# Kernel tuning notes

Measured on AMD Instinct MI355X. Metric: run time of the kernel, lower is better.

Reference implementation:

```python
import jax, jax.numpy as jnp
import numpy as np

GRID = 8
S = GRID * GRID          # 64 tokens
D = 256                  # embed dim
H = 4                    # heads
HD = D // H              # 64 head dim
L = 8                    # depth
EPS = 1.1920929e-07      # torch.finfo(float32).eps (nn.RMSNorm eps=None)
RADIUS = 2.5


def _grid_coords():
    y, x = np.meshgrid(np.arange(GRID), np.arange(GRID), indexing='ij')
    return np.stack([y.ravel(), x.ravel()], axis=1).astype(np.float32)  # [S,2]


def _rope_cos_sin():
    coords = _grid_coords()
    dim_half = HD // 2  # 32
    inv_freq = 1.0 / (10000.0 ** (np.arange(0, dim_half, 2, dtype=np.float32) / dim_half))  # [16]
    fy = coords[:, 0:1] * inv_freq[None, :]   # [S,16]
    fx = coords[:, 1:2] * inv_freq[None, :]   # [S,16]
    freqs = np.concatenate([fy, fx], axis=-1)  # [S,32]
    emb = np.concatenate([freqs, freqs], axis=-1)  # [S,64]
    return jnp.asarray(np.cos(emb)), jnp.asarray(np.sin(emb))


def _local_mask():
    coords = _grid_coords()
    d = np.sqrt(((coords[:, None, :] - coords[None, :, :]) ** 2).sum(-1))
    return jnp.asarray(d < RADIUS)  # [S,S] bool


COS, SIN = _rope_cos_sin()
MASK_LOCAL = _local_mask()
MASK_GLOBAL = jnp.ones((S, S), dtype=bool)


def rms(x):
    return x * jax.lax.rsqrt(jnp.mean(x * x, axis=-1, keepdims=True) + EPS)


def householder_Q(vs):
    # vs: [R, HD]; Q = prod of reflections applied as in the torch loop
    def step(Q, v):
        vn = jnp.sum(v * v) + 1e-08
        return Q - (2.0 / vn) * jnp.outer(v, v @ Q), None
    Q, _ = jax.lax.scan(step, jnp.eye(HD, dtype=vs.dtype), vs)
    return Q


def rotate_half(x):
    x1, x2 = jnp.split(x, 2, axis=-1)
    return jnp.concatenate([-x2, x1], axis=-1)


def block(x, vs_l, wqkv, wout, wg, bg, wmg, bmg, wmo, bmo, mask):
    B = x.shape[0]
    xn = rms(x)
    qkv = xn @ wqkv                                # [B,S,3D]
    q, k, v = jnp.split(qkv, 3, axis=-1)
    q = q.reshape(B, S, H, HD).transpose(0, 2, 1, 3)   # [B,H,S,HD]
    k = k.reshape(B, S, H, HD).transpose(0, 2, 1, 3)
    v = v.reshape(B, S, H, HD).transpose(0, 2, 1, 3)
    Q = householder_Q(vs_l)                        # [HD,HD]
    # inverse rotation, standard RoPE, forward rotation
    q = q @ Q.T
    k = k @ Q.T
    cos = COS[None, None]                          # [1,1,S,HD]
    sin = SIN[None, None]
    q = q * cos + rotate_half(q) * sin
    k = k * cos + rotate_half(k) * sin
    q = q @ Q
    k = k @ Q
    scores = jnp.einsum('bhqd,bhkd->bhqk', q, k) / jnp.sqrt(jnp.float32(HD))
    scores = jnp.where(mask[None, None], scores, -jnp.inf)
    attn = jax.nn.softmax(scores, axis=-1)
    out = jnp.einsum('bhqk,bhkd->bhqd', attn, v)   # [B,H,S,HD]
    out = out.transpose(0, 2, 1, 3).reshape(B, S, D)
    out = out @ wout
    gate = jax.nn.sigmoid(out @ wg + bg)
    x = x + out * gate
    xn = rms(x)
    m = xn @ wmg + bmg                             # [B,S,8D]
    g, val = jnp.split(m, 2, axis=-1)
    x = x + (val * jax.nn.gelu(g, approximate=False)) @ wmo + bmo
    return x


def setup_inputs() -> dict:
    key = jax.random.key(0)
    ks = jax.random.split(key, 20)
    B = 1024
    s = 0.02
    return {
        'z_t': jax.random.normal(ks[0], (B, 3, 16, 16), jnp.float32),
        'logsnr': jax.random.normal(ks[1], (B,), jnp.float32),
        'w_patch_in': jax.random.normal(ks[2], (20, D), jnp.float32) * s,
        'b_patch_in': jnp.zeros((D,), jnp.float32),
        'vs': jax.random.normal(ks[3], (L, HD // 2, HD), jnp.float32) * s,
        'w_qkv': jax.random.normal(ks[4], (L, D, 3 * D), jnp.float32) * s,
        'w_out': jax.random.normal(ks[5], (L, D, D), jnp.float32) * s,
        'w_gate': jax.random.normal(ks[6], (L, D, D), jnp.float32) * s,
        'b_gate': jnp.zeros((L, D), jnp.float32),
        'w_mlp_gate': jax.random.normal(ks[7], (L, D, 8 * D), jnp.float32) * s,
        'b_mlp_gate': jnp.zeros((L, 8 * D), jnp.float32),
        'w_mlp_out': jax.random.normal(ks[8], (L, 4 * D, D), jnp.float32) * s,
        'b_mlp_out': jnp.zeros((L, D), jnp.float32),
        'norm_final_w': jnp.ones((D,), jnp.float32),
        'w_head': jax.random.normal(ks[9], (D, D), jnp.float32) * s,
        'b_head': jnp.zeros((D,), jnp.float32),
        'w_patch_out': jax.random.normal(ks[10], (D, 12), jnp.float32) * s,
        'b_patch_out': jnp.zeros((12,), jnp.float32),
    }


def reference(z_t, logsnr, w_patch_in, b_patch_in, vs, w_qkv, w_out, w_gate, b_gate,
              w_mlp_gate, b_mlp_gate, w_mlp_out, b_mlp_out, norm_final_w,
              w_head, b_head, w_patch_out, b_patch_out):
    B = z_t.shape[0]
    # patchify: [B,3,16,16] -> [B,64,12] (2x2 patches over 8x8 grid)
    patches = z_t.reshape(B, 3, GRID, 2, GRID, 2).transpose(0, 2, 4, 1, 3, 5).reshape(B, S, 12)
    # Fourier features of logsnr: num_bands=4, max_range=40
    freqs = (2.0 * np.pi / 40.0) * (2.0 ** jnp.arange(4, dtype=jnp.float32))
    args = logsnr[:, None] * freqs                 # [B,4]
    spins = jnp.concatenate([jnp.sin(args), jnp.cos(args)], axis=-1)  # [B,8]
    spins = jnp.broadcast_to(spins[:, None, :], (B, S, 8))
    x = jnp.concatenate([patches, spins], axis=-1) @ w_patch_in + b_patch_in  # [B,S,D]
    for i in range(L):
        mask = MASK_GLOBAL if (i + 1) % 4 == 0 else MASK_LOCAL
        x = block(x, vs[i], w_qkv[i], w_out[i], w_gate[i], b_gate[i],
                  w_mlp_gate[i], b_mlp_gate[i], w_mlp_out[i], b_mlp_out[i], mask)
    x = rms(x) * norm_final_w
    out = x @ w_head + b_head
    z = out @ w_patch_out + b_patch_out            # [B,S,12]
    z = z.reshape(B, GRID, GRID, 3, 2, 2).transpose(0, 3, 1, 4, 2, 5).reshape(B, 3, 16, 16)
    return z
```

## Files before the change

kernel.cpp:

```cpp
#include <hip/hip_runtime.h>

#define DEV static __device__ __forceinline__

typedef float f32x4 __attribute__((ext_vector_type(4)));
typedef short s16x8 __attribute__((ext_vector_type(8)));
typedef __bf16 bf16x8 __attribute__((ext_vector_type(8)));

DEV unsigned short f2bf(float f) {
  union { float f; unsigned u; } v; v.f = f;
  unsigned r = v.u + 0x7FFFu + ((v.u >> 16) & 1u);
  return (unsigned short)(r >> 16);
}
DEV float bf2f(unsigned short h) {
  union { unsigned u; float f; } v; v.u = ((unsigned)h) << 16;
  return v.f;
}
DEV void g2l16(const void* g, void* l) {
  __builtin_amdgcn_global_load_lds((const __attribute__((address_space(1))) void*)g,
                                   (__attribute__((address_space(3))) void*)l, 16, 0, 0);
}
DEV f32x4 mfma16(bf16x8 a, bf16x8 b, f32x4 c) {
  return __builtin_amdgcn_mfma_f32_16x16x32_bf16(a, b, c, 0, 0, 0);
}
DEV int xcd_swz(int bid, int nwg) {
  return (bid & 7) * (nwg >> 3) + (bid >> 3);
}
DEV float gelu_t(float g) {
  float y = 0.7978845608028654f * (g + 0.044715f * g * g * g);
  float th = 1.f - 2.f * __builtin_amdgcn_rcpf(1.f + __expf(2.f * y));
  return 0.5f * g * (1.f + th);
}

__global__ void k_house(const float* __restrict__ VS, float* __restrict__ Qg) {
  const int l = blockIdx.x, t = threadIdx.x;
  float Qc[64];
#pragma unroll
  for (int i = 0; i < 64; i++) Qc[i] = (i == t) ? 1.f : 0.f;
  for (int rr = 0; rr < 32; rr++) {
    float vt = VS[(size_t)l * 2048 + rr * 64 + t];
    float vn = vt * vt;
#pragma unroll
    for (int o = 1; o < 64; o <<= 1) vn += __shfl_xor(vn, o, 64);
    float vv[64];
#pragma unroll
    for (int i = 0; i < 64; i++) vv[i] = __shfl(vt, i, 64);
    float w0 = 0.f, w1 = 0.f, w2 = 0.f, w3 = 0.f;
#pragma unroll
    for (int i = 0; i < 64; i += 4) {
      w0 = fmaf(vv[i + 0], Qc[i + 0], w0);
      w1 = fmaf(vv[i + 1], Qc[i + 1], w1);
      w2 = fmaf(vv[i + 2], Qc[i + 2], w2);
      w3 = fmaf(vv[i + 3], Qc[i + 3], w3);
    }
    float c = (2.f / (vn + 1e-8f)) * ((w0 + w1) + (w2 + w3));
#pragma unroll
    for (int i = 0; i < 64; i++) Qc[i] = fmaf(-vv[i], c, Qc[i]);
  }
#pragma unroll
  for (int i = 0; i < 64; i++) Qg[(size_t)l * 4096 + i * 64 + t] = Qc[i];
}

__global__ void k_rope(float* __restrict__ C, float* __restrict__ Sn) {
  int idx = blockIdx.x * 256 + threadIdx.x;
  if (idx >= 4096) return;
  int s = idx >> 6, d = idx & 63;
  int dh = d & 31;
  float coord = (dh < 16) ? (float)(s >> 3) : (float)(s & 7);
  int fi = dh & 15;
  float invf = powf(10000.f, -(float)fi / 16.f);
  float ang = coord * invf;
  C[idx] = cosf(ang);
  Sn[idx] = sinf(ang);
}

__global__ __launch_bounds__(256) void k_fold_qkv(const float* __restrict__ W,
                                                  const float* __restrict__ Qg,
                                                  unsigned short* __restrict__ out) {
  __shared__ float qrows[16 * 64];
  __shared__ float tr[16 * 256];
  const int l = blockIdx.x / 48, ng = blockIdx.x % 48;
  const int n0 = ng * 16, t = threadIdx.x;
  const float* Wl = W + (size_t)l * 256 * 768;
  float res[16];
  if (n0 < 512) {
    int part = n0 >> 8, h = (n0 & 255) >> 6, j0 = n0 & 63;
    for (int i = t; i < 1024; i += 256) {
      int jj = i >> 6, dd = i & 63;
      qrows[i] = Qg[(size_t)l * 4096 + (j0 + jj) * 64 + dd];
    }
    __syncthreads();
    const float* wrow = Wl + (size_t)t * 768 + part * 256 + h * 64;
    float wreg[64];
    for (int d = 0; d < 64; d++) wreg[d] = wrow[d];
    for (int jj = 0; jj < 16; jj++) {
      float a = 0.f;
      for (int d = 0; d < 64; d++) a += wreg[d] * qrows[jj * 64 + d];
      res[jj] = a;
    }
  } else {
    for (int jj = 0; jj < 16; jj++) res[jj] = Wl[(size_t)t * 768 + n0 + jj];
    __syncthreads();
  }
  __syncthreads();
  for (int jj = 0; jj < 16; jj++) tr[jj * 256 + t] = res[jj];
  __syncthreads();
  size_t base = (size_t)l * 196608 + (size_t)(n0 >> 4) * 4096;
  int kb = t >> 3, jn0 = (t & 7) * 2;
  s16x8 w0, w1;
  for (int u = 0; u < 8; u++) w0[u] = (short)f2bf(tr[jn0 * 256 + kb * 8 + u]);
  for (int u = 0; u < 8; u++) w1[u] = (short)f2bf(tr[(jn0 + 1) * 256 + kb * 8 + u]);
  *(s16x8*)(out + base + (size_t)t * 16) = w0;
  *(s16x8*)(out + base + (size_t)t * 16 + 8) = w1;
}

__global__ __launch_bounds__(256) void k_fold_w2(const float* __restrict__ WO,
                                                 const float* __restrict__ WG,
                                                 unsigned short* __restrict__ out) {
  __shared__ float wgs[256 * 16];
  __shared__ float tr[16 * 256];
  const int l = blockIdx.x >> 5, ng = blockIdx.x & 31;
  const int n0 = ng * 16, t = threadIdx.x;
  const float* WOl = WO + (size_t)l * 65536;
  float res[16];
  if (n0 < 256) {
    for (int jj = 0; jj < 16; jj++) res[jj] = WOl[(size_t)t * 256 + n0 + jj];
  } else {
    int c0 = n0 - 256;
    const float* WGl = WG + (size_t)l * 65536;
    for (int i = t; i < 4096; i += 256) {
      int k = i >> 4, c = i & 15;
      wgs[i] = WGl[(size_t)k * 256 + c0 + c];
    }
    __syncthreads();
    float a[16];
    for (int c = 0; c < 16; c++) a[c] = 0.f;
    for (int k = 0; k < 256; k++) {
      float wo = WOl[(size_t)t * 256 + k];
      for (int c = 0; c < 16; c++) a[c] += wo * wgs[k * 16 + c];
    }
    for (int c = 0; c < 16; c++) res[c] = a[c];
  }
  __syncthreads();
  for (int jj = 0; jj < 16; jj++) tr[jj * 256 + t] = res[jj];
  __syncthreads();
  size_t base = (size_t)l * 131072 + (size_t)(n0 >> 4) * 4096;
  int kb = t >> 3, jn0 = (t & 7) * 2;
  s16x8 w0, w1;
  for (int u = 0; u < 8; u++) w0[u] = (short)f2bf(tr[jn0 * 256 + kb * 8 + u]);
  for (int u = 0; u < 8; u++) w1[u] = (short)f2bf(tr[(jn0 + 1) * 256 + kb * 8 + u]);
  *(s16x8*)(out + base + (size_t)t * 16) = w0;
  *(s16x8*)(out + base + (size_t)t * 16 + 8) = w1;
}

__global__ __launch_bounds__(256) void k_conv_wmg(const float* __restrict__ W,
                                                  unsigned short* __restrict__ out) {
  __shared__ float tr[16 * 256];
  const int l = blockIdx.x >> 7, ng = blockIdx.x & 127;
  const int n0 = ng * 16, t = threadIdx.x;
  const float* src = W + (size_t)l * 256 * 2048 + (size_t)t * 2048 + n0;
  for (int j = 0; j < 16; j++) tr[j * 256 + t] = src[j];
  __syncthreads();
  size_t base = (size_t)l * 524288 + (size_t)ng * 4096;
  int kb = t >> 3, jn0 = (t & 7) * 2;
  s16x8 w0, w1;
  for (int u = 0; u < 8; u++) w0[u] = (short)f2bf(tr[jn0 * 256 + kb * 8 + u]);
  for (int u = 0; u < 8; u++) w1[u] = (short)f2bf(tr[(jn0 + 1) * 256 + kb * 8 + u]);
  *(s16x8*)(out + base + (size_t)t * 16) = w0;
  *(s16x8*)(out + base + (size_t)t * 16 + 8) = w1;
}

__global__ __launch_bounds__(256) void k_conv_wmo(const float* __restrict__ W,
                                                  unsigned short* __restrict__ out) {
  __shared__ float tr[16 * 256];
  const int l = blockIdx.x >> 4, ng = blockIdx.x & 15;
  const int n0 = ng * 16, t = threadIdx.x;
  const float* Wl = W + (size_t)l * 1024 * 256;
  size_t base = (size_t)l * 262144 + (size_t)ng * 16384;
  for (int c4 = 0; c4 < 4; c4++) {
    int k0 = c4 * 256;
    for (int j = 0; j < 16; j++) tr[j * 256 + t] = Wl[(size_t)(k0 + t) * 256 + n0 + j];
    __syncthreads();
    int kb = t >> 3, jn0 = (t & 7) * 2;
    s16x8 w0, w1;
    for (int u = 0; u < 8; u++) w0[u] = (short)f2bf(tr[jn0 * 256 + kb * 8 + u]);
    for (int u = 0; u < 8; u++) w1[u] = (short)f2bf(tr[(jn0 + 1) * 256 + kb * 8 + u]);
    *(s16x8*)(out + base + (size_t)(k0 >> 3) * 128 + (size_t)t * 16) = w0;
    *(s16x8*)(out + base + (size_t)(k0 >> 3) * 128 + (size_t)t * 16 + 8) = w1;
    __syncthreads();
  }
}

__global__ __launch_bounds__(256) void k_fold_head(const float* __restrict__ WH,
                                                   const float* __restrict__ BH,
                                                   const float* __restrict__ WPO,
                                                   const float* __restrict__ BPO,
                                                   float* __restrict__ WHP,
                                                   float* __restrict__ BHP) {
  __shared__ float wpos[256 * 12];
  const int t = threadIdx.x;
  for (int i = t; i < 3072; i += 256) wpos[i] = WPO[i];
  __syncthreads();
  float a[12];
  for (int c = 0; c < 12; c++) a[c] = 0.f;
  const float* whrow = WH + (size_t)t * 256;
  for (int k = 0; k < 256; k++) {
    float w = whrow[k];
    for (int c = 0; c < 12; c++) a[c] += w * wpos[k * 12 + c];
  }
  for (int c = 0; c < 12; c++) WHP[t * 12 + c] = a[c];
  if (t < 12) {
    float b = BPO[t];
    for (int k = 0; k < 256; k++) b += BH[k] * wpos[k * 12 + t];
    BHP[t] = b;
  }
}

__global__ __launch_bounds__(256) void k_embed(const float* __restrict__ ZT,
                                               const float* __restrict__ LOGSNR,
                                               const float* __restrict__ WPI,
                                               const float* __restrict__ BPI,
                                               float* __restrict__ X) {
  __shared__ float zb[768];
  __shared__ float sp[8];
  const int b = blockIdx.x, t = threadIdx.x;
  for (int i = t; i < 768; i += 256) zb[i] = ZT[(size_t)b * 768 + i];
  if (t < 8) {
    float freq = 0.15707963267948966f * (float)(1 << (t & 3));
    float a = LOGSNR[b] * freq;
    sp[t] = (t < 4) ? sinf(a) : cosf(a);
  }
  __syncthreads();
  float wc[20];
  for (int j = 0; j < 20; j++) wc[j] = WPI[j * 256 + t];
  float bk = BPI[t];
  for (int s = 0; s < 64; s++) {
    int gy = s >> 3, gx = s & 7;
    float acc = bk;
    for (int j = 0; j < 12; j++) {
      int cch = j >> 2, py = (j >> 1) & 1, px = j & 1;
      acc += zb[cch * 256 + (gy * 2 + py) * 16 + gx * 2 + px] * wc[j];
    }
    for (int j = 0; j < 8; j++) acc += sp[j] * wc[12 + j];
    X[((size_t)b * 64 + s) * 256 + t] = acc;
  }
}

__global__ __launch_bounds__(256) void k_rms(const float* __restrict__ X,
                                             unsigned short* __restrict__ XN) {
  const int m0 = blockIdx.x * 16, t = threadIdx.x;
  const int r = t >> 4, cj = t & 15;
  const float* row = X + (size_t)(m0 + r) * 256 + cj * 16;
  float4 a = *(const float4*)(row);
  float4 b = *(const float4*)(row + 4);
  float4 c = *(const float4*)(row + 8);
  float4 d = *(const float4*)(row + 12);
  float ss = a.x * a.x + a.y * a.y + a.z * a.z + a.w * a.w +
             b.x * b.x + b.y * b.y + b.z * b.z + b.w * b.w +
             c.x * c.x + c.y * c.y + c.z * c.z + c.w * c.w +
             d.x * d.x + d.y * d.y + d.z * d.z + d.w * d.w;
  for (int o = 1; o < 16; o <<= 1) ss += __shfl_xor(ss, o, 64);
  float rq = rsqrtf(ss * (1.f / 256.f) + 1.1920929e-07f);
  s16x8 v0, v1;
  v0[0] = (short)f2bf(a.x * rq); v0[1] = (short)f2bf(a.y * rq);
  v0[2] = (short)f2bf(a.z * rq); v0[3] = (short)f2bf(a.w * rq);
  v0[4] = (short)f2bf(b.x * rq); v0[5] = (short)f2bf(b.y * rq);
  v0[6] = (short)f2bf(b.z * rq); v0[7] = (short)f2bf(b.w * rq);
  v1[0] = (short)f2bf(c.x * rq); v1[1] = (short)f2bf(c.y * rq);
  v1[2] = (short)f2bf(c.z * rq); v1[3] = (short)f2bf(c.w * rq);
  v1[4] = (short)f2bf(d.x * rq); v1[5] = (short)f2bf(d.y * rq);
  v1[6] = (short)f2bf(d.z * rq); v1[7] = (short)f2bf(d.w * rq);
  size_t base = ((size_t)blockIdx.x * 32 + cj * 2) * 128 + r * 8;
  *(s16x8*)(XN + base) = v0;
  *(s16x8*)(XN + base + 128) = v1;
}

template <int KD, int NT, int MODE>
__global__ __launch_bounds__(256) void k_gemm_single(const unsigned short* __restrict__ A,
                                                     const unsigned short* __restrict__ Bw,
                                                     unsigned short* __restrict__ Cout,
                                                     const float* __restrict__ bias,
                                                     float* __restrict__ X) {
  __shared__ unsigned short sm[17408];
  unsigned short* la = sm;
  unsigned short* lb = sm + 4096;
  const int t = threadIdx.x;
  const int lane = t & 63, wv = t >> 6;
  const int swz = xcd_swz(blockIdx.x, gridDim.x);
  const int bm = swz / NT, bn = swz % NT;
  const int m0 = bm * 128, n0 = bn * 128;
  const int wm = wv >> 1, wn = wv & 1;
  constexpr int KB8 = KD >> 3;

  f32x4 acc[4][4];
  f32x4 zz = {0.f, 0.f, 0.f, 0.f};
  for (int i = 0; i < 4; i++)
    for (int j = 0; j < 4; j++) acc[i][j] = zz;

  for (int k0 = 0; k0 < KD; k0 += 32) {
    const int kb0 = k0 >> 3;
    for (int ii = 0; ii < 2; ii++) {
      size_t mg = (size_t)(m0 >> 4) + ii * 4 + wv;
      g2l16(A + (mg * KB8 + kb0) * 128 + lane * 8, la + (ii * 4 + wv) * 512 + lane * 8);
    }
    for (int ii = 0; ii < 2; ii++) {
      size_t ng = (size_t)(n0 >> 4) + ii * 4 + wv;
      g2l16(Bw + (ng * KB8 + kb0) * 128 + lane * 8, lb + (ii * 4 + wv) * 512 + lane * 8);
    }
    __syncthreads();
    bf16x8 af[4], bb[4];
    for (int i = 0; i < 4; i++) af[i] = *(const bf16x8*)(la + (wm * 4 + i) * 512 + lane * 8);
    for (int j = 0; j < 4; j++) bb[j] = *(const bf16x8*)(lb + (wn * 4 + j) * 512 + lane * 8);
    for (int i = 0; i < 4; i++)
      for (int j = 0; j < 4; j++) acc[i][j] = mfma16(af[i], bb[j], acc[i][j]);
    __syncthreads();
  }

  const int lr = lane & 15, lg = lane >> 4;
  if constexpr (MODE == 0) {
    unsigned short* lc = sm;
    for (int i = 0; i < 4; i++)
      for (int j = 0; j < 4; j++)
        for (int e = 0; e < 4; e++) {
          int r = wm * 64 + i * 16 + lg * 4 + e;
          int c = wn * 64 + j * 16 + lr;
          lc[r * 136 + c] = f2bf(acc[i][j][e]);
        }
    __syncthreads();
    for (int p = 0; p < 8; p++) {
      int r = p * 16 + (t >> 4);
      int c = (t & 15) * 8;
      *(s16x8*)(Cout + (size_t)(m0 + r) * (NT * 128) + n0 + c) = *(const s16x8*)(lc + r * 136 + c);
    }
  } else {
    for (int i = 0; i < 4; i++)
      for (int j = 0; j < 4; j++) {
        int c = n0 + wn * 64 + j * 16 + lr;
        float bv = bias[c];
        for (int e = 0; e < 4; e++) {
          int r = m0 + wm * 64 + i * 16 + lg * 4 + e;
          X[(size_t)r * 256 + c] += acc[i][j][e] + bv;
        }
      }
  }
}

template <int KD, int MODE>
__global__ __launch_bounds__(256) void k_gemm_dual(const unsigned short* __restrict__ A,
                                                   const unsigned short* __restrict__ B0,
                                                   const unsigned short* __restrict__ B1,
                                                   const float* __restrict__ bias,
                                                   float* __restrict__ X,
                                                   unsigned short* __restrict__ Hout,
                                                   int NT) {
  __shared__ unsigned short sm[9216];
  unsigned short* la = sm;
  unsigned short* lb0 = sm + 4096;
  unsigned short* lb1 = sm + 6144;
  const int t = threadIdx.x, lane = t & 63, wv = t >> 6;
  const int swz = xcd_swz(blockIdx.x, gridDim.x);
  const int bm = swz / NT, bn = swz % NT;
  const int m0 = bm * 128, n0 = bn * 64;
  constexpr int KB8 = KD >> 3;
  f32x4 acc0[2][4], acc1[2][4];
  f32x4 zz = {0.f, 0.f, 0.f, 0.f};
  for (int i = 0; i < 2; i++)
    for (int j = 0; j < 4; j++) { acc0[i][j] = zz; acc1[i][j] = zz; }

  for (int k0 = 0; k0 < KD; k0 += 32) {
    const int kb0 = k0 >> 3;
    for (int ii = 0; ii < 2; ii++) {
      size_t mg = (size_t)(m0 >> 4) + ii * 4 + wv;
      g2l16(A + (mg * KB8 + kb0) * 128 + lane * 8, la + (ii * 4 + wv) * 512 + lane * 8);
    }
    size_t ng = (size_t)(n0 >> 4) + wv;
    g2l16(B0 + (ng * KB8 + kb0) * 128 + lane * 8, lb0 + wv * 512 + lane * 8);
    g2l16(B1 + (ng * KB8 + kb0) * 128 + lane * 8, lb1 + wv * 512 + lane * 8);
    __syncthreads();
    bf16x8 af[2];
    for (int i = 0; i < 2; i++) af[i] = *(const bf16x8*)(la + (wv * 2 + i) * 512 + lane * 8);
    for (int j = 0; j < 4; j++) {
      bf16x8 b0 = *(const bf16x8*)(lb0 + j * 512 + lane * 8);
      bf16x8 b1 = *(const bf16x8*)(lb1 + j * 512 + lane * 8);
      for (int i = 0; i < 2; i++) {
        acc0[i][j] = mfma16(af[i], b0, acc0[i][j]);
        acc1[i][j] = mfma16(af[i], b1, acc1[i][j]);
      }
    }
    __syncthreads();
  }

  const int lr = lane & 15, lg = lane >> 4;
  if constexpr (MODE == 0) {
    for (int i = 0; i < 2; i++)
      for (int j = 0; j < 4; j++) {
        int c = n0 + j * 16 + lr;
        float bv = bias[c];
        for (int e = 0; e < 4; e++) {
          int r = m0 + wv * 32 + i * 16 + lg * 4 + e;
          float o = acc0[i][j][e];
          float g = acc1[i][j][e] + bv;
          X[(size_t)r * 256 + c] += o * __builtin_amdgcn_rcpf(1.f + __expf(-g));
        }
      }
  } else {
    unsigned short* lc = sm;
    for (int i = 0; i < 2; i++)
      for (int j = 0; j < 4; j++) {
        int cl = j * 16 + lr;
        float bg_ = bias[n0 + cl];
        float bv_ = bias[1024 + n0 + cl];
        for (int e = 0; e < 4; e++) {
          int rl = wv * 32 + i * 16 + lg * 4 + e;
          float g = acc0[i][j][e] + bg_;
          float vv = acc1[i][j][e] + bv_;
          lc[rl * 72 + cl] = f2bf(vv * gelu_t(g));
        }
      }
    __syncthreads();
    for (int it = 0; it < 4; it++) {
      int idx = it * 2048 + t * 8;
      int mg_l = idx >> 10, rem = idx & 1023;
      int kb_l = rem >> 7, r = (rem >> 3) & 15;
      *(s16x8*)(Hout + ((size_t)((m0 >> 4) + mg_l) * 128 + (n0 >> 3) + kb_l) * 128 + r * 8) =
          *(const s16x8*)(lc + (mg_l * 16 + r) * 72 + kb_l * 8);
    }
  }
}

__global__ __launch_bounds__(256) void k_attn(const unsigned short* __restrict__ QKV,
                                              const float* __restrict__ CT,
                                              const float* __restrict__ ST,
                                              unsigned short* __restrict__ AO,
                                              int use_local) {
  __shared__ unsigned short sm[16384];
  unsigned short* qs = sm;
  unsigned short* ks = sm + 4096;
  unsigned short* vt = sm + 8192;
  unsigned short* ps = sm + 12288;
  const int blk = blockIdx.x;
  const int b = blk >> 2, h = blk & 3;
  const int t = threadIdx.x, lane = t & 63, wv = t >> 6;
  const size_t rowbase = (size_t)b * 64 * 768;

  {
    int s = t >> 2, dq = (t & 3) * 8;
    const unsigned short* qrow = QKV + rowbase + (size_t)s * 768 + h * 64;
    s16x8 qlo = *(const s16x8*)(qrow + dq);
    s16x8 qhi = *(const s16x8*)(qrow + dq + 32);
    s16x8 klo = *(const s16x8*)(qrow + 256 + dq);
    s16x8 khi = *(const s16x8*)(qrow + 256 + dq + 32);
    s16x8 oql, oqh, okl, okh;
    for (int e = 0; e < 8; e++) {
      float cl = CT[s * 64 + dq + e], sl = ST[s * 64 + dq + e];
      float ch = CT[s * 64 + dq + 32 + e], sh = ST[s * 64 + dq + 32 + e];
      float ql = bf2f((unsigned short)qlo[e]), qh = bf2f((unsigned short)qhi[e]);
      oql[e] = (short)f2bf((ql * cl - qh * sl) * 0.125f);
      oqh[e] = (short)f2bf((qh * ch + ql * sh) * 0.125f);
      float kl = bf2f((unsigned short)klo[e]), kh = bf2f((unsigned short)khi[e]);
      okl[e] = (short)f2bf(kl * cl - kh * sl);
      okh[e] = (short)f2bf(kh * ch + kl * sh);
    }
    int off_lo = (((s >> 4) * 8 + (dq >> 3)) * 16 + (s & 15)) * 8;
    int off_hi = (((s >> 4) * 8 + (dq >> 3) + 4) * 16 + (s & 15)) * 8;
    *(s16x8*)(qs + off_lo) = oql;
    *(s16x8*)(qs + off_hi) = oqh;
    *(s16x8*)(ks + off_lo) = okl;
    *(s16x8*)(ks + off_hi) = okh;
    int d0 = (t & 3) * 16;
    s16x8 v0 = *(const s16x8*)(qrow + 512 + d0);
    s16x8 v1 = *(const s16x8*)(qrow + 512 + d0 + 8);
    for (int e = 0; e < 8; e++) {
      int d = d0 + e;
      vt[(((d >> 4) * 8 + (s >> 3)) * 16 + (d & 15)) * 8 + (s & 7)] = (unsigned short)v0[e];
      d = d0 + 8 + e;
      vt[(((d >> 4) * 8 + (s >> 3)) * 16 + (d & 15)) * 8 + (s & 7)] = (unsigned short)v1[e];
    }
  }
  __syncthreads();

  f32x4 sc[4];
  f32x4 zz = {0.f, 0.f, 0.f, 0.f};
  for (int j = 0; j < 4; j++) sc[j] = zz;
  for (int kk = 0; kk < 2; kk++) {
    bf16x8 aq = *(const bf16x8*)(qs + wv * 1024 + kk * 512 + lane * 8);
    for (int j = 0; j < 4; j++)
      sc[j] = mfma16(aq, *(const bf16x8*)(ks + j * 1024 + kk * 512 + lane * 8), sc[j]);
  }

  const int lr = lane & 15, lg = lane >> 4;
  for (int e = 0; e < 4; e++) {
    int sq = wv * 16 + lg * 4 + e;
    int yq = sq >> 3, xq = sq & 7;
    float mx = -1e30f;
    float vals[4];
    for (int j = 0; j < 4; j++) {
      int sk = j * 16 + lr;
      float v = sc[j][e];
      if (use_local) {
        int dy = yq - (sk >> 3), dx = xq - (sk & 7);
        if (dy * dy + dx * dx > 6) v = -1e30f;
      }
      vals[j] = v;
      mx = fmaxf(mx, v);
    }
    for (int o = 1; o < 16; o <<= 1) mx = fmaxf(mx, __shfl_xor(mx, o, 64));
    float sum = 0.f;
    for (int j = 0; j < 4; j++) {
      float p = __expf(vals[j] - mx);
      vals[j] = p;
      sum += p;
    }
    for (int o = 1; o < 16; o <<= 1) sum += __shfl_xor(sum, o, 64);
    float inv = __builtin_amdgcn_rcpf(sum);
    for (int j = 0; j < 4; j++) {
      int sk = j * 16 + lr;
      ps[((wv * 8 + (sk >> 3)) * 16 + (sq & 15)) * 8 + (sk & 7)] = f2bf(vals[j] * inv);
    }
  }
  __syncthreads();

  f32x4 oa[4];
  for (int j = 0; j < 4; j++) oa[j] = zz;
  for (int kk = 0; kk < 2; kk++) {
    bf16x8 ap = *(const bf16x8*)(ps + wv * 1024 + kk * 512 + lane * 8);
    for (int j = 0; j < 4; j++)
      oa[j] = mfma16(ap, *(const bf16x8*)(vt + j * 1024 + kk * 512 + lane * 8), oa[j]);
  }
  unsigned short* os = qs + wv * 1024;
  for (int j = 0; j < 4; j++)
    for (int e = 0; e < 4; e++) os[(lg * 4 + e) * 64 + j * 16 + lr] = f2bf(oa[j][e]);
  __syncthreads();
  const size_t obase = ((size_t)(b * 4 + wv) * 32 + h * 8) * 128;
  for (int c = 0; c < 2; c++) {
    int idx = c * 64 + lane;
    int kb = idx >> 4, r = idx & 15;
    *(s16x8*)(AO + obase + (size_t)kb * 128 + r * 8) = *(const s16x8*)(os + r * 64 + kb * 8);
  }
}

__global__ __launch_bounds__(256) void k_head(const float* __restrict__ X,
                                              const float* __restrict__ NW,
                                              const float* __restrict__ WHP,
                                              const float* __restrict__ BHP,
                                              float* __restrict__ OUT) {
  __shared__ float wh[256 * 12];
  __shared__ float nw[256];
  __shared__ float bh[12];
  const int b = blockIdx.x, t = threadIdx.x;
  for (int i = t; i < 3072; i += 256) wh[i] = WHP[i];
  nw[t] = NW[t];
  if (t < 12) bh[t] = BHP[t];
  __syncthreads();
  const int r = t >> 2, qd = t & 3;
  const float* row = X + ((size_t)b * 64 + r) * 256 + qd * 64;
  float ss = 0.f;
  for (int i = 0; i < 64; i++) ss += row[i] * row[i];
  ss += __shfl_xor(ss, 1, 64);
  ss += __shfl_xor(ss, 2, 64);
  float rq = rsqrtf(ss * (1.f / 256.f) + 1.1920929e-07f);
  float accs[12];
  for (int c = 0; c < 12; c++) accs[c] = 0.f;
  for (int i = 0; i < 64; i++) {
    float xf = row[i] * rq * nw[qd * 64 + i];
    const float* wr = wh + (qd * 64 + i) * 12;
    for (int c = 0; c < 12; c++) accs[c] += xf * wr[c];
  }
  for (int c = 0; c < 12; c++) {
    accs[c] += __shfl_xor(accs[c], 1, 64);
    accs[c] += __shfl_xor(accs[c], 2, 64);
  }
  int gy = r >> 3, gx = r & 7;
  for (int u = 0; u < 3; u++) {
    int c = qd * 3 + u;
    float val = accs[c] + bh[c];
    int ch = c >> 2, py = (c >> 1) & 1, px = c & 1;
    OUT[(size_t)b * 768 + ch * 256 + (gy * 2 + py) * 16 + (gx * 2 + px)] = val;
  }
}

extern "C" void kernel_launch(void* const* d_in, const int* in_sizes, int n_in,
                              void* d_out, int out_size, void* d_ws, size_t ws_size,
                              hipStream_t stream) {
  (void)n_in; (void)out_size; (void)ws_size;
  const float* z_t    = (const float*)d_in[0];
  const float* logsnr = (const float*)d_in[1];
  const float* wpi    = (const float*)d_in[2];
  const float* bpi    = (const float*)d_in[3];
  const float* vs     = (const float*)d_in[4];
  const float* wqkv   = (const float*)d_in[5];
  const float* wout   = (const float*)d_in[6];
  const float* wgate  = (const float*)d_in[7];
  const float* bgate  = (const float*)d_in[8];
  const float* wmg    = (const float*)d_in[9];
  const float* bmg    = (const float*)d_in[10];
  const float* wmo    = (const float*)d_in[11];
  const float* bmo    = (const float*)d_in[12];
  const float* nfw    = (const float*)d_in[13];
  const float* whead  = (const float*)d_in[14];
  const float* bhead  = (const float*)d_in[15];
  const float* wpo    = (const float*)d_in[16];
  const float* bpo    = (const float*)d_in[17];
  float* OUT = (float*)d_out;

  const int Bn = in_sizes[0] / 768;
  const int Mtot = Bn * 64;

  char* w = (char*)d_ws;
  auto alloc = [&](size_t bytes) {
    char* p = w;
    w += (bytes + 255) & ~(size_t)255;
    return p;
  };
  float* Qg  = (float*)alloc((size_t)8 * 4096 * 4);
  float* Ct  = (float*)alloc(4096 * 4);
  float* St  = (float*)alloc(4096 * 4);
  float* WHP = (float*)alloc(3072 * 4);
  float* BHP = (float*)alloc(64);
  unsigned short* WqkvS = (unsigned short*)alloc((size_t)8 * 768 * 256 * 2);
  unsigned short* W2S   = (unsigned short*)alloc((size_t)8 * 512 * 256 * 2);
  unsigned short* WmgS  = (unsigned short*)alloc((size_t)8 * 2048 * 256 * 2);
  unsigned short* WmoS  = (unsigned short*)alloc((size_t)8 * 256 * 1024 * 2);
  float* X = (float*)alloc((size_t)Mtot * 256 * 4);
  unsigned short* XN  = (unsigned short*)alloc((size_t)Mtot * 256 * 2);
  unsigned short* BIG = (unsigned short*)alloc((size_t)Mtot * 1024 * 2);
  unsigned short* QKVb = BIG;
  unsigned short* AOb  = BIG + (size_t)Mtot * 768;
  unsigned short* Hb   = BIG;

  k_house<<<8, 64, 0, stream>>>(vs, Qg);
  k_rope<<<16, 256, 0, stream>>>(Ct, St);
  k_fold_qkv<<<8 * 48, 256, 0, stream>>>(wqkv, Qg, WqkvS);
  k_fold_w2<<<8 * 32, 256, 0, stream>>>(wout, wgate, W2S);
  k_conv_wmg<<<8 * 128, 256, 0, stream>>>(wmg, WmgS);
  k_conv_wmo<<<8 * 16, 256, 0, stream>>>(wmo, WmoS);
  k_fold_head<<<1, 256, 0, stream>>>(whead, bhead, wpo, bpo, WHP, BHP);
  k_embed<<<Bn, 256, 0, stream>>>(z_t, logsnr, wpi, bpi, X);

  for (int l = 0; l < 8; l++) {
    k_rms<<<Mtot / 16, 256, 0, stream>>>(X, XN);
    k_gemm_single<256, 6, 0><<<(Mtot / 128) * 6, 256, 0, stream>>>(
        XN, WqkvS + (size_t)l * 196608, QKVb, nullptr, nullptr);
    k_attn<<<Bn * 4, 256, 0, stream>>>(QKVb, Ct, St, AOb, ((l + 1) % 4) ? 1 : 0);
    k_gemm_dual<256, 0><<<(Mtot / 128) * 4, 256, 0, stream>>>(
        AOb, W2S + (size_t)l * 131072, W2S + (size_t)l * 131072 + 65536,
        bgate + l * 256, X, nullptr, 4);
    k_rms<<<Mtot / 16, 256, 0, stream>>>(X, XN);
    k_gemm_dual<256, 1><<<(Mtot / 128) * 16, 256, 0, stream>>>(
        XN, WmgS + (size_t)l * 524288, WmgS + (size_t)l * 524288 + 262144,
        bmg + l * 2048, nullptr, Hb, 16);
    k_gemm_single<1024, 2, 1><<<(Mtot / 128) * 2, 256, 0, stream>>>(
        Hb, WmoS + (size_t)l * 262144, nullptr, bmo + l * 256, X);
  }
  k_head<<<Bn, 256, 0, stream>>>(X, nfw, WHP, BHP, OUT);
}
```

Measured before the change: 2.671 ms.

## Double K-step in dual GEMM and stage residual epilogues through LDS

The dual GEMM main loop now loads 64 K elements per iteration instead of 32, with larger LDS buffers, so the number of barriers per tile is halved. The residual-add epilogues of both the single GEMM and the dual GEMM first write results into LDS. They then do coalesced float4 read-modify-write into X instead of scattered scalar updates. This costs more shared memory, which may lower occupancy, and adds extra barriers in the epilogue.

```diff
diff --git a/kernel.cpp b/kernel.cpp
--- a/kernel.cpp
+++ b/kernel.cpp
@@ -332,15 +332,31 @@
       *(s16x8*)(Cout + (size_t)(m0 + r) * (NT * 128) + n0 + c) = *(const s16x8*)(lc + r * 136 + c);
     }
   } else {
-    for (int i = 0; i < 4; i++)
-      for (int j = 0; j < 4; j++) {
-        int c = n0 + wn * 64 + j * 16 + lr;
-        float bv = bias[c];
-        for (int e = 0; e < 4; e++) {
-          int r = m0 + wm * 64 + i * 16 + lg * 4 + e;
-          X[(size_t)r * 256 + c] += acc[i][j][e] + bv;
-        }
+    float* lcf = (float*)sm;
+    for (int p = 0; p < 2; p++) {
+      if (wm == p) {
+        for (int i = 0; i < 4; i++)
+          for (int j = 0; j < 4; j++) {
+            int c = wn * 64 + j * 16 + lr;
+            float bv = bias[n0 + c];
+            for (int e = 0; e < 4; e++) {
+              int rr = i * 16 + lg * 4 + e;
+              lcf[rr * 132 + c] = acc[i][j][e] + bv;
+            }
+          }
       }
+      __syncthreads();
+      for (int k = 0; k < 8; k++) {
+        int q = t + 256 * k;
+        int row = q >> 5, col4 = q & 31;
+        float* xp = X + (size_t)(m0 + p * 64 + row) * 256 + n0 + col4 * 4;
+        float4 xv = *(float4*)xp;
+        const float* lp = lcf + row * 132 + col4 * 4;
+        xv.x += lp[0]; xv.y += lp[1]; xv.z += lp[2]; xv.w += lp[3];
+        *(float4*)xp = xv;
+      }
+      __syncthreads();
+    }
   }
 }
 
@@ -352,10 +368,11 @@
                                                    float* __restrict__ X,
                                                    unsigned short* __restrict__ Hout,
                                                    int NT) {
-  __shared__ unsigned short sm[9216];
+  constexpr int SMSH = (MODE == 0) ? 17408 : 16384;
+  __shared__ unsigned short sm[SMSH];
   unsigned short* la = sm;
-  unsigned short* lb0 = sm + 4096;
-  unsigned short* lb1 = sm + 6144;
+  unsigned short* lb0 = sm + 8192;
+  unsigned short* lb1 = sm + 12288;
   const int t = threadIdx.x, lane = t & 63, wv = t >> 6;
   const int swz = xcd_swz(blockIdx.x, gridDim.x);
   const int bm = swz / NT, bn = swz % NT;
@@ -366,24 +383,39 @@
   for (int i = 0; i < 2; i++)
     for (int j = 0; j < 4; j++) { acc0[i][j] = zz; acc1[i][j] = zz; }
 
-  for (int k0 = 0; k0 < KD; k0 += 32) {
+  for (int k0 = 0; k0 < KD; k0 += 64) {
     const int kb0 = k0 >> 3;
+#pragma unroll
+    for (int ii = 0; ii < 4; ii++) {
+      int task = ii * 4 + wv;
+      int mg = task >> 1, g = task & 1;
+      g2l16(A + ((size_t)((m0 >> 4) + mg) * KB8 + kb0 + g * 4) * 128 + lane * 8,
+            la + task * 512 + lane * 8);
+    }
+#pragma unroll
     for (int ii = 0; ii < 2; ii++) {
-      size_t mg = (size_t)(m0 >> 4) + ii * 4 + wv;
-      g2l16(A + (mg * KB8 + kb0) * 128 + lane * 8, la + (ii * 4 + wv) * 512 + lane * 8);
-    }
-    size_t ng = (size_t)(n0 >> 4) + wv;
-    g2l16(B0 + (ng * KB8 + kb0) * 128 + lane * 8, lb0 + wv * 512 + lane * 8);
-    g2l16(B1 + (ng * KB8 + kb0) * 128 + lane * 8, lb1 + wv * 512 + lane * 8);
-    __syncthreads();
-    bf16x8 af[2];
-    for (int i = 0; i < 2; i++) af[i] = *(const bf16x8*)(la + (wv * 2 + i) * 512 + lane * 8);
-    for (int j = 0; j < 4; j++) {
-      bf16x8 b0 = *(const bf16x8*)(lb0 + j * 512 + lane * 8);
-      bf16x8 b1 = *(const bf16x8*)(lb1 + j * 512 + lane * 8);
-      for (int i = 0; i < 2; i++) {
-        acc0[i][j] = mfma16(af[i], b0, acc0[i][j]);
-        acc1[i][j] = mfma16(af[i], b1, acc1[i][j]);
+      int task = ii * 4 + wv;
+      int ng = task >> 1, g = task & 1;
+      size_t srcoff = ((size_t)((n0 >> 4) + ng) * KB8 + kb0 + g * 4) * 128 + lane * 8;
+      g2l16(B0 + srcoff, lb0 + task * 512 + lane * 8);
+      g2l16(B1 + srcoff, lb1 + task * 512 + lane * 8);
+    }
+    __syncthreads();
+#pragma unroll
+    for (int kk = 0; kk < 2; kk++) {
+      bf16x8 af[2];
+#pragma unroll
+      for (int i = 0; i < 2; i++)
+        af[i] = *(const bf16x8*)(la + ((wv * 2 + i) * 8 + kk * 4) * 128 + lane * 8);
+#pragma unroll
+      for (int j = 0; j < 4; j++) {
+        bf16x8 b0 = *(const bf16x8*)(lb0 + (j * 8 + kk * 4) * 128 + lane * 8);
+        bf16x8 b1 = *(const bf16x8*)(lb1 + (j * 8 + kk * 4) * 128 + lane * 8);
+#pragma unroll
+        for (int i = 0; i < 2; i++) {
+          acc0[i][j] = mfma16(af[i], b0, acc0[i][j]);
+          acc1[i][j] = mfma16(af[i], b1, acc1[i][j]);
+        }
       }
     }
     __syncthreads();
@@ -391,17 +423,28 @@
 
   const int lr = lane & 15, lg = lane >> 4;
   if constexpr (MODE == 0) {
+    float* lcf = (float*)sm;
     for (int i = 0; i < 2; i++)
       for (int j = 0; j < 4; j++) {
-        int c = n0 + j * 16 + lr;
-        float bv = bias[c];
+        int c = j * 16 + lr;
+        float bv = bias[n0 + c];
         for (int e = 0; e < 4; e++) {
-          int r = m0 + wv * 32 + i * 16 + lg * 4 + e;
+          int r = wv * 32 + i * 16 + lg * 4 + e;
           float o = acc0[i][j][e];
           float g = acc1[i][j][e] + bv;
-          X[(size_t)r * 256 + c] += o * __builtin_amdgcn_rcpf(1.f + __expf(-g));
+          lcf[r * 68 + c] = o * __builtin_amdgcn_rcpf(1.f + __expf(-g));
         }
       }
+    __syncthreads();
+    for (int k = 0; k < 8; k++) {
+      int q = t + 256 * k;
+      int row = q >> 4, col4 = q & 15;
+      float* xp = X + (size_t)(m0 + row) * 256 + n0 + col4 * 4;
+      float4 xv = *(float4*)xp;
+      const float* lp = lcf + row * 68 + col4 * 4;
+      xv.x += lp[0]; xv.y += lp[1]; xv.z += lp[2]; xv.w += lp[3];
+      *(float4*)xp = xv;
+    }
   } else {
     unsigned short* lc = sm;
     for (int i = 0; i < 2; i++)
```

Result: slower. 2.832 ms (+6.1%).
